# Optimization experiments

Hardware: AMD Instinct MI355X
Metric: run time of the kernel (lower is better)

The kernel has to match this reference:

```python
import jax, jax.numpy as jnp
import numpy as np

DIM = 1024
N_HEADS = 16
HEAD_DIM = DIM // N_HEADS


def setup_inputs() -> dict:
    key = jax.random.key(0)
    ks = jax.random.split(key, 5)
    scale = 1.0 / np.sqrt(DIM)
    x = jax.random.normal(ks[0], (2, 2048, DIM), dtype=jnp.float32)
    W_qkv = jax.random.normal(ks[1], (DIM, 3 * DIM), dtype=jnp.float32) * scale
    b_qkv = jax.random.normal(ks[2], (3 * DIM,), dtype=jnp.float32) * 0.01
    W_proj = jax.random.normal(ks[3], (DIM, DIM), dtype=jnp.float32) * scale
    b_proj = jax.random.normal(ks[4], (DIM,), dtype=jnp.float32) * 0.01
    return {"x": x, "W_qkv": W_qkv, "b_qkv": b_qkv, "W_proj": W_proj, "b_proj": b_proj}


def reference(x, W_qkv, b_qkv, W_proj, b_proj):
    B, T, C = x.shape
    qkv = x @ W_qkv + b_qkv  # [B,T,3C]
    q, k, v = jnp.split(qkv, 3, axis=2)
    # [B,T,C] -> [B,H,T,Dh]
    def heads(y):
        return y.reshape(B, T, N_HEADS, HEAD_DIM).transpose(0, 2, 1, 3)
    q, k, v = heads(q), heads(k), heads(v)
    inv_sqrt_dh = 1.0 / jnp.sqrt(jnp.asarray(HEAD_DIM, dtype=x.dtype))
    attn = jnp.einsum('bhqd,bhkd->bhqk', q, k) * inv_sqrt_dh
    attn = jax.nn.softmax(attn, axis=-1)
    out = jnp.einsum('bhqk,bhkd->bhqd', attn, v)
    out = out.transpose(0, 2, 1, 3).reshape(B, T, C)
    return out @ W_proj + b_proj
```

## Files before the change

kernel.cpp:

```cpp
#include <hip/hip_runtime.h>
#include <hip/hip_bf16.h>
#include <math.h>

using bf16 = __hip_bfloat16;

typedef __bf16 bf16x8 __attribute__((ext_vector_type(8)));
typedef __bf16 bf16x4 __attribute__((ext_vector_type(4)));
typedef float  f32x4  __attribute__((ext_vector_type(4)));
typedef float  f32x16 __attribute__((ext_vector_type(16)));

constexpr int Bb = 2;
constexpr int Ts = 2048;
constexpr int Cc = 1024;
constexpr int Hh = 16;
constexpr int Dh = 64;
constexpr int Mm = Bb * Ts;
constexpr int Nqkv = 3 * Cc;
constexpr int BHTD = Bb * Hh * Ts * Dh;

__device__ __forceinline__
void gll16(const __bf16* g, __bf16* l)
{
    __builtin_amdgcn_global_load_lds(
        (const __attribute__((address_space(1))) unsigned int*)g,
        (__attribute__((address_space(3))) unsigned int*)l,
        16, 0, 0);
}

__global__ __launch_bounds__(256)
void prep_all(const float* __restrict__ x, __bf16* __restrict__ Xb,
              const float* __restrict__ Wq, __bf16* __restrict__ Wqt,
              const float* __restrict__ Wp, __bf16* __restrict__ Wpt)
{
    __shared__ __bf16 tl[64][72];
    const int bid = blockIdx.x;
    const int t = threadIdx.x;

    if (bid < 4096) {
        int i = (bid * 256 + t) * 4;
        float4 v = *(const float4*)(x + i);
        bf16x4 o = { (__bf16)v.x, (__bf16)v.y, (__bf16)v.z, (__bf16)v.w };
        *(bf16x4*)(Xb + i) = o;
        return;
    }
    const float* W; __bf16* Wt; int cols, bx, by;
    if (bid < 4096 + 768) {
        W = Wq; Wt = Wqt; cols = Nqkv;
        bx = (bid - 4096) % 48; by = (bid - 4096) / 48;
    } else {
        W = Wp; Wt = Wpt; cols = Cc;
        bx = (bid - 4864) % 16; by = (bid - 4864) / 16;
    }
    const int c0 = bx * 64;
    const int r0 = by * 64;
    #pragma unroll
    for (int i = 0; i < 4; i++) {
        int e = t + 256 * i;
        int r = e >> 4, c4 = (e & 15) * 4;
        float4 v = *(const float4*)(W + (r0 + r) * cols + c0 + c4);
        bf16x4 o = { (__bf16)v.x, (__bf16)v.y, (__bf16)v.z, (__bf16)v.w };
        *(bf16x4*)&tl[r][c4] = o;
    }
    __syncthreads();
    #pragma unroll
    for (int i = 0; i < 4; i++) {
        int e = t + 256 * i;
        int n = e >> 4, k4 = (e & 15) * 4;
        bf16x4 o = { tl[k4][n], tl[k4 + 1][n], tl[k4 + 2][n], tl[k4 + 3][n] };
        *(bf16x4*)(Wt + (c0 + n) * 1024 + r0 + k4) = o;
    }
}

__device__ __forceinline__
void gemm_core(const __bf16* __restrict__ A, const __bf16* __restrict__ Bt,
               int m0, int n0, int wm, int wn, int quad, int l16, int t,
               f32x4 (&acc)[4][4])
{
    __shared__ __bf16 Al[128][32];
    __shared__ __bf16 Bl[128][32];

    const int wave = t >> 6;
    const int lane = t & 63;
    const int srow = lane >> 2;
    const int scol = (lane & 3) * 8;

    const __bf16* Ag = A  + (size_t)(m0 + wave * 16 + srow) * 1024 + scol;
    const __bf16* Bg = Bt + (size_t)(n0 + wave * 16 + srow) * 1024 + scol;
    __bf16* Al_lo = &Al[wave * 16][0];
    __bf16* Al_hi = &Al[64 + wave * 16][0];
    __bf16* Bl_lo = &Bl[wave * 16][0];
    __bf16* Bl_hi = &Bl[64 + wave * 16][0];

    for (int k0 = 0; k0 < 1024; k0 += 32) {
        gll16(Ag + k0,             Al_lo);
        gll16(Ag + k0 + 64 * 1024, Al_hi);
        gll16(Bg + k0,             Bl_lo);
        gll16(Bg + k0 + 64 * 1024, Bl_hi);
        __syncthreads();
        bf16x8 af[4], bfr[4];
        #pragma unroll
        for (int mt = 0; mt < 4; mt++)
            af[mt] = *(const bf16x8*)&Al[wm * 64 + mt * 16 + l16][quad * 8];
        #pragma unroll
        for (int nt = 0; nt < 4; nt++)
            bfr[nt] = *(const bf16x8*)&Bl[wn * 64 + nt * 16 + l16][quad * 8];
        #pragma unroll
        for (int mt = 0; mt < 4; mt++)
            #pragma unroll
            for (int nt = 0; nt < 4; nt++)
                acc[mt][nt] = __builtin_amdgcn_mfma_f32_16x16x32_bf16(
                    af[mt], bfr[nt], acc[mt][nt], 0, 0, 0);
        __syncthreads();
    }
}

__global__ __launch_bounds__(256)
void qkv_mfma(const __bf16* __restrict__ A, const __bf16* __restrict__ Bt,
              const float* __restrict__ bias, __bf16* __restrict__ qkv)
{
    __shared__ __bf16 ebuf[4][64][72];

    const int t    = threadIdx.x;
    const int wave = t >> 6;
    const int lane = t & 63;
    const int quad = lane >> 4;
    const int l16  = lane & 15;
    const int wm   = wave >> 1, wn = wave & 1;
    const int n0 = blockIdx.x * 128;
    const int m0 = blockIdx.y * 128;

    f32x4 acc[4][4];
    #pragma unroll
    for (int i = 0; i < 4; i++)
        #pragma unroll
        for (int j = 0; j < 4; j++)
            acc[i][j] = f32x4{0.f, 0.f, 0.f, 0.f};

    gemm_core(A, Bt, m0, n0, wm, wn, quad, l16, t, acc);

    const int nw0 = n0 + wn * 64;
    const int which = nw0 >> 10;
    const int h = (nw0 & 1023) >> 6;

    if (which == 2) {
        #pragma unroll
        for (int nt = 0; nt < 4; nt++) {
            int d = nt * 16 + l16;
            float bs = bias[nw0 + nt * 16 + l16];
            #pragma unroll
            for (int mt = 0; mt < 4; mt++) {
                int m = m0 + wm * 64 + mt * 16 + quad * 4;
                int b = m >> 11;
                int tt = m & 2047;
                bf16x4 o = { (__bf16)(acc[mt][nt][0] + bs),
                             (__bf16)(acc[mt][nt][1] + bs),
                             (__bf16)(acc[mt][nt][2] + bs),
                             (__bf16)(acc[mt][nt][3] + bs) };
                *(bf16x4*)&qkv[2 * (size_t)BHTD +
                               (((size_t)(b * 16 + h) * 64 + d) * 2048 + tt)] = o;
            }
        }
    } else {
        #pragma unroll
        for (int nt = 0; nt < 4; nt++) {
            float bs = bias[nw0 + nt * 16 + l16];
            #pragma unroll
            for (int mt = 0; mt < 4; mt++)
                #pragma unroll
                for (int r = 0; r < 4; r++)
                    ebuf[wave][mt * 16 + quad * 4 + r][nt * 16 + l16] =
                        (__bf16)(acc[mt][nt][r] + bs);
        }
        int m = m0 + wm * 64 + lane;
        int b = m >> 11;
        int tt = m & 2047;
        __bf16* dst = &qkv[which * (size_t)BHTD +
                           (((size_t)(b * 16 + h) * 2048 + tt) * 64)];
        #pragma unroll
        for (int c = 0; c < 8; c++)
            *(bf16x8*)(dst + c * 8) = *(const bf16x8*)&ebuf[wave][lane][c * 8];
    }
}

__global__ __launch_bounds__(256)
void proj_mfma(const __bf16* __restrict__ A, const __bf16* __restrict__ Bt,
               const float* __restrict__ bias, float* __restrict__ out)
{
    const int t    = threadIdx.x;
    const int wave = t >> 6;
    const int lane = t & 63;
    const int quad = lane >> 4;
    const int l16  = lane & 15;
    const int wm   = wave >> 1, wn = wave & 1;
    const int n0 = blockIdx.x * 128;
    const int m0 = blockIdx.y * 128;

    f32x4 acc[4][4];
    #pragma unroll
    for (int i = 0; i < 4; i++)
        #pragma unroll
        for (int j = 0; j < 4; j++)
            acc[i][j] = f32x4{0.f, 0.f, 0.f, 0.f};

    gemm_core(A, Bt, m0, n0, wm, wn, quad, l16, t, acc);

    #pragma unroll
    for (int nt = 0; nt < 4; nt++) {
        int n = n0 + wn * 64 + nt * 16 + l16;
        float bs = bias[n];
        #pragma unroll
        for (int mt = 0; mt < 4; mt++) {
            #pragma unroll
            for (int r = 0; r < 4; r++) {
                int m = m0 + wm * 64 + mt * 16 + quad * 4 + r;
                out[m * 1024 + n] = acc[mt][nt][r] + bs;
            }
        }
    }
}

__global__ __launch_bounds__(256, 1)
void attn_mfma(const __bf16* __restrict__ Q, const __bf16* __restrict__ K,
               const __bf16* __restrict__ VT, __bf16* __restrict__ O)
{
    __shared__ __bf16 sK[2][64 * 64];
    __shared__ __bf16 sV[2][64 * 64];

    const int t    = threadIdx.x;
    const int wave = t >> 6;
    const int lane = t & 63;
    const int c    = lane & 31;
    const int hi   = lane >> 5;
    const int hx   = hi * 16;
    const int sw   = (c & 7) << 4;

    const int blk = blockIdx.x;
    const int bh  = blk & 31;
    const int qc  = blk >> 5;
    const int q0  = qc * 256 + wave * 64;

    const __bf16* Qp = Q  + ((size_t)bh * Ts + q0) * Dh;
    const __bf16* Kp = K  + (size_t)bh * Ts * Dh;
    const __bf16* Vp = VT + (size_t)bh * Dh * Ts;

    bf16x8 qf[2][4];
    #pragma unroll
    for (int qs = 0; qs < 2; qs++)
        #pragma unroll
        for (int ds = 0; ds < 4; ds++) {
            bf16x8 v = *(const bf16x8*)(Qp + (qs * 32 + c) * Dh + ds * 16 + hi * 8);
            #pragma unroll
            for (int i = 0; i < 8; i++) v[i] = (__bf16)(0.125f * (float)v[i]);
            qf[qs][ds] = v;
        }

    f32x16 accO[2][2];
    #pragma unroll
    for (int qs = 0; qs < 2; qs++)
        #pragma unroll
        for (int dt = 0; dt < 2; dt++)
            #pragma unroll
            for (int i = 0; i < 16; i++) accO[qs][dt][i] = 0.f;
    float lsum[2] = {0.f, 0.f};

    const int r0 = wave * 8 + (lane >> 3);
    const int s8 = ((lane & 7) ^ (r0 & 7)) * 8;
    const __bf16* kg0 = Kp + r0 * Dh + s8;
    const __bf16* kg1 = Kp + (size_t)(32 + r0) * Dh + s8;
    const __bf16* vg0 = Vp + (size_t)r0 * Ts + s8;
    const __bf16* vg1 = Vp + (size_t)(32 + r0) * Ts + s8;

    gll16(kg0, &sK[0][wave * 512]);
    gll16(kg1, &sK[0][2048 + wave * 512]);
    gll16(vg0, &sV[0][wave * 512]);
    gll16(vg1, &sV[0][2048 + wave * 512]);
    __syncthreads();

    for (int ic = 0; ic < Ts / 64; ic++) {
        const int p = ic & 1;
        if (ic < Ts / 64 - 1) {
            const int pn = p ^ 1;
            gll16(kg0 + (ic + 1) * 4096, &sK[pn][wave * 512]);
            gll16(kg1 + (ic + 1) * 4096, &sK[pn][2048 + wave * 512]);
            gll16(vg0 + (ic + 1) * 64,   &sV[pn][wave * 512]);
            gll16(vg1 + (ic + 1) * 64,   &sV[pn][2048 + wave * 512]);
        }
        const char* kb = (const char*)&sK[p][0];
        const char* vb = (const char*)&sV[p][0];

        bf16x8 kf[2][4];
        #pragma unroll
        for (int kt = 0; kt < 2; kt++) {
            const char* rbase = kb + (kt * 32 + c) * 128;
            #pragma unroll
            for (int ds = 0; ds < 4; ds++)
                kf[kt][ds] = *(const bf16x8*)(rbase + ((ds * 32 + hx) ^ sw));
        }

        f32x16 st[2][2];
        #pragma unroll
        for (int qs = 0; qs < 2; qs++)
            #pragma unroll
            for (int kt = 0; kt < 2; kt++)
                #pragma unroll
                for (int i = 0; i < 16; i++) st[qs][kt][i] = 0.f;
        #pragma unroll
        for (int ds = 0; ds < 4; ds++)
            #pragma unroll
            for (int kt = 0; kt < 2; kt++)
                #pragma unroll
                for (int qs = 0; qs < 2; qs++)
                    st[qs][kt] = __builtin_amdgcn_mfma_f32_32x32x16_bf16(
                        kf[kt][ds], qf[qs][ds], st[qs][kt], 0, 0, 0);

        bf16x8 pa[2][4];
        #pragma unroll
        for (int qs = 0; qs < 2; qs++) {
            unsigned pk[2][8];
            #pragma unroll
            for (int kt = 0; kt < 2; kt++) {
                float sum0 = 0.f, sum1 = 0.f;
                #pragma unroll
                for (int r = 0; r < 16; r++) {
                    float pv = __expf(st[qs][kt][r]);
                    st[qs][kt][r] = pv;
                    if (r & 1) sum1 += pv; else sum0 += pv;
                }
                lsum[qs] += sum0 + sum1;
                #pragma unroll
                for (int r2 = 0; r2 < 8; r2++) {
                    unsigned d;
                    asm("v_cvt_pk_bf16_f32 %0, %1, %2"
                        : "=v"(d)
                        : "v"(st[qs][kt][2 * r2]), "v"(st[qs][kt][2 * r2 + 1]));
                    pk[kt][r2] = d;
                }
            }
            #pragma unroll
            for (int s = 0; s < 4; s++) {
                const int kt = s >> 1, r4 = (s & 1) * 4;
                unsigned x0 = pk[kt][r4 + 0], y0 = pk[kt][r4 + 2];
                unsigned x1 = pk[kt][r4 + 1], y1 = pk[kt][r4 + 3];
                asm("v_permlane32_swap_b32 %0, %1" : "+v"(x0), "+v"(y0));
                asm("v_permlane32_swap_b32 %0, %1" : "+v"(x1), "+v"(y1));
                union { unsigned u[4]; bf16x8 b; } pu;
                pu.u[0] = x0; pu.u[1] = x1; pu.u[2] = y0; pu.u[3] = y1;
                pa[qs][s] = pu.b;
            }
        }

        #pragma unroll
        for (int s = 0; s < 4; s++)
            #pragma unroll
            for (int dt = 0; dt < 2; dt++) {
                bf16x8 vf = *(const bf16x8*)(vb + (dt * 32 + c) * 128 +
                                             ((s * 32 + hx) ^ sw));
                #pragma unroll
                for (int qs = 0; qs < 2; qs++)
                    accO[qs][dt] = __builtin_amdgcn_mfma_f32_32x32x16_bf16(
                        pa[qs][s], vf, accO[qs][dt], 0, 0, 0);
            }
        __syncthreads();
    }

    const int b = bh >> 4, h = bh & 15;
    #pragma unroll
    for (int qs = 0; qs < 2; qs++) {
        float l = lsum[qs] + __shfl_xor(lsum[qs], 32);
        float linv = 1.f / l;
        #pragma unroll
        for (int r = 0; r < 16; r++) {
            const int qrow = (r & 3) + 8 * (r >> 2) + 4 * hi;
            float inv = __shfl(linv, qrow);
            __bf16* Op = O + ((size_t)(b * Ts + q0 + qs * 32 + qrow)) * Cc +
                         h * 64 + c;
            Op[0]  = (__bf16)(accO[qs][0][r] * inv);
            Op[32] = (__bf16)(accO[qs][1][r] * inv);
        }
    }
}

extern "C" void kernel_launch(void* const* d_in, const int* in_sizes, int n_in,
                              void* d_out, int out_size, void* d_ws, size_t ws_size,
                              hipStream_t stream)
{
    (void)in_sizes; (void)n_in; (void)out_size; (void)ws_size;
    const float* x     = (const float*)d_in[0];
    const float* Wqkv  = (const float*)d_in[1];
    const float* bqkv  = (const float*)d_in[2];
    const float* Wproj = (const float*)d_in[3];
    const float* bproj = (const float*)d_in[4];
    float* out = (float*)d_out;

    __bf16* ws   = (__bf16*)d_ws;
    __bf16* Qw   = ws;
    __bf16* XbAO = ws + 3 * (size_t)BHTD;
    __bf16* Wqt  = XbAO + (size_t)Mm * Cc;
    __bf16* Wpt  = Wqt + (size_t)Nqkv * Cc;

    prep_all<<<dim3(5120), 256, 0, stream>>>(x, XbAO, Wqkv, Wqt, Wproj, Wpt);
    qkv_mfma<<<dim3(Nqkv / 128, Mm / 128), 256, 0, stream>>>(XbAO, Wqt, bqkv, Qw);
    attn_mfma<<<dim3(256), 256, 0, stream>>>(
        Qw, Qw + BHTD, Qw + 2 * (size_t)BHTD, XbAO);
    proj_mfma<<<dim3(Cc / 128, Mm / 128), 256, 0, stream>>>(XbAO, Wpt, bproj, out);
}
```

Before: 207.7 us.

## Register-pipeline attention K/V loads from global, shrink proj tile to 64 rows

Attention no longer stages K and V through double-buffered LDS. Each wave now loads K/V fragments straight from global into registers and runs a software-pipelined loop that overlaps the QK, softmax and PV stages across even and odd key blocks. Softmax switches to exp2 with log2e folded into the Q scale, and the per-iteration barriers are removed. The projection GEMM uses 64-row M tiles to double the block count. The trade-off is that each of the four waves now reads K/V from global or L2 on its own instead of sharing one LDS copy, and register pressure rises.

Result: no change. 205.4 us (-1.1%).

```diff
diff --git a/kernel.cpp b/kernel.cpp
--- a/kernel.cpp
+++ b/kernel.cpp
@@ -71,14 +71,16 @@
     }
 }
 
+template<int BM>
 __device__ __forceinline__
 void gemm_core(const __bf16* __restrict__ A, const __bf16* __restrict__ Bt,
                int m0, int n0, int wm, int wn, int quad, int l16, int t,
                f32x4 (&acc)[4][4])
 {
-    __shared__ __bf16 Al[128][32];
+    __shared__ __bf16 Al[BM][32];
     __shared__ __bf16 Bl[128][32];
 
+    constexpr int MT = BM / 32;
     const int wave = t >> 6;
     const int lane = t & 63;
     const int srow = lane >> 2;
@@ -87,25 +89,27 @@
     const __bf16* Ag = A  + (size_t)(m0 + wave * 16 + srow) * 1024 + scol;
     const __bf16* Bg = Bt + (size_t)(n0 + wave * 16 + srow) * 1024 + scol;
     __bf16* Al_lo = &Al[wave * 16][0];
-    __bf16* Al_hi = &Al[64 + wave * 16][0];
     __bf16* Bl_lo = &Bl[wave * 16][0];
     __bf16* Bl_hi = &Bl[64 + wave * 16][0];
 
     for (int k0 = 0; k0 < 1024; k0 += 32) {
-        gll16(Ag + k0,             Al_lo);
-        gll16(Ag + k0 + 64 * 1024, Al_hi);
+        gll16(Ag + k0, Al_lo);
+        if constexpr (BM == 128) {
+            __bf16* Al_hi = &Al[64 + wave * 16][0];
+            gll16(Ag + k0 + 64 * 1024, Al_hi);
+        }
         gll16(Bg + k0,             Bl_lo);
         gll16(Bg + k0 + 64 * 1024, Bl_hi);
         __syncthreads();
-        bf16x8 af[4], bfr[4];
-        #pragma unroll
-        for (int mt = 0; mt < 4; mt++)
-            af[mt] = *(const bf16x8*)&Al[wm * 64 + mt * 16 + l16][quad * 8];
+        bf16x8 af[MT], bfr[4];
+        #pragma unroll
+        for (int mt = 0; mt < MT; mt++)
+            af[mt] = *(const bf16x8*)&Al[wm * (BM / 2) + mt * 16 + l16][quad * 8];
         #pragma unroll
         for (int nt = 0; nt < 4; nt++)
             bfr[nt] = *(const bf16x8*)&Bl[wn * 64 + nt * 16 + l16][quad * 8];
         #pragma unroll
-        for (int mt = 0; mt < 4; mt++)
+        for (int mt = 0; mt < MT; mt++)
             #pragma unroll
             for (int nt = 0; nt < 4; nt++)
                 acc[mt][nt] = __builtin_amdgcn_mfma_f32_16x16x32_bf16(
@@ -136,7 +140,7 @@
         for (int j = 0; j < 4; j++)
             acc[i][j] = f32x4{0.f, 0.f, 0.f, 0.f};
 
-    gemm_core(A, Bt, m0, n0, wm, wn, quad, l16, t, acc);
+    gemm_core<128>(A, Bt, m0, n0, wm, wn, quad, l16, t, acc);
 
     const int nw0 = n0 + wn * 64;
     const int which = nw0 >> 10;
@@ -193,7 +197,7 @@
     const int l16  = lane & 15;
     const int wm   = wave >> 1, wn = wave & 1;
     const int n0 = blockIdx.x * 128;
-    const int m0 = blockIdx.y * 128;
+    const int m0 = blockIdx.y * 64;
 
     f32x4 acc[4][4];
     #pragma unroll
@@ -202,47 +206,129 @@
         for (int j = 0; j < 4; j++)
             acc[i][j] = f32x4{0.f, 0.f, 0.f, 0.f};
 
-    gemm_core(A, Bt, m0, n0, wm, wn, quad, l16, t, acc);
+    gemm_core<64>(A, Bt, m0, n0, wm, wn, quad, l16, t, acc);
 
     #pragma unroll
     for (int nt = 0; nt < 4; nt++) {
         int n = n0 + wn * 64 + nt * 16 + l16;
         float bs = bias[n];
         #pragma unroll
-        for (int mt = 0; mt < 4; mt++) {
+        for (int mt = 0; mt < 2; mt++) {
             #pragma unroll
             for (int r = 0; r < 4; r++) {
-                int m = m0 + wm * 64 + mt * 16 + quad * 4 + r;
+                int m = m0 + wm * 32 + mt * 16 + quad * 4 + r;
                 out[m * 1024 + n] = acc[mt][nt][r] + bs;
             }
         }
     }
+}
+
+__device__ __forceinline__
+void ldk_g(const __bf16* __restrict__ Kb, int j, bf16x8 (&kf)[2][4])
+{
+    #pragma unroll
+    for (int kt = 0; kt < 2; kt++)
+        #pragma unroll
+        for (int ds = 0; ds < 4; ds++)
+            kf[kt][ds] = *(const bf16x8*)(Kb + ((size_t)j * 64 + kt * 32) * 64 + ds * 16);
+}
+
+__device__ __forceinline__
+void ldv_g(const __bf16* __restrict__ Vb, int j, bf16x8 (&vf)[4][2])
+{
+    #pragma unroll
+    for (int s = 0; s < 4; s++)
+        #pragma unroll
+        for (int dt = 0; dt < 2; dt++)
+            vf[s][dt] = *(const bf16x8*)(Vb + (size_t)dt * 32 * Ts + j * 64 + s * 16);
+}
+
+__device__ __forceinline__
+void qk_step(const bf16x8 (&kf)[2][4], const bf16x8 (&qf)[2][4], f32x16 (&st)[2][2])
+{
+    const f32x16 z16 = {0.f, 0.f, 0.f, 0.f, 0.f, 0.f, 0.f, 0.f,
+                        0.f, 0.f, 0.f, 0.f, 0.f, 0.f, 0.f, 0.f};
+    #pragma unroll
+    for (int kt = 0; kt < 2; kt++)
+        #pragma unroll
+        for (int qs = 0; qs < 2; qs++) {
+            f32x16 a;
+            a = __builtin_amdgcn_mfma_f32_32x32x16_bf16(kf[kt][0], qf[qs][0], z16, 0, 0, 0);
+            a = __builtin_amdgcn_mfma_f32_32x32x16_bf16(kf[kt][1], qf[qs][1], a, 0, 0, 0);
+            a = __builtin_amdgcn_mfma_f32_32x32x16_bf16(kf[kt][2], qf[qs][2], a, 0, 0, 0);
+            st[qs][kt] = __builtin_amdgcn_mfma_f32_32x32x16_bf16(kf[kt][3], qf[qs][3], a, 0, 0, 0);
+        }
+}
+
+__device__ __forceinline__
+void sm_step(f32x16 (&st)[2][2], bf16x8 (&pa)[2][4], float (&lsum)[2])
+{
+    #pragma unroll
+    for (int qs = 0; qs < 2; qs++) {
+        #pragma unroll
+        for (int kt = 0; kt < 2; kt++) {
+            float sum0 = 0.f, sum1 = 0.f;
+            #pragma unroll
+            for (int r = 0; r < 16; r++) {
+                float pv = __builtin_amdgcn_exp2f(st[qs][kt][r]);
+                st[qs][kt][r] = pv;
+                if (r & 1) sum1 += pv; else sum0 += pv;
+            }
+            lsum[qs] += sum0 + sum1;
+            #pragma unroll
+            for (int s2 = 0; s2 < 2; s2++) {
+                unsigned pk0, pk1, pk2, pk3;
+                const int r4 = s2 * 8;
+                asm("v_cvt_pk_bf16_f32 %0, %1, %2"
+                    : "=v"(pk0) : "v"(st[qs][kt][r4 + 0]), "v"(st[qs][kt][r4 + 1]));
+                asm("v_cvt_pk_bf16_f32 %0, %1, %2"
+                    : "=v"(pk1) : "v"(st[qs][kt][r4 + 2]), "v"(st[qs][kt][r4 + 3]));
+                asm("v_cvt_pk_bf16_f32 %0, %1, %2"
+                    : "=v"(pk2) : "v"(st[qs][kt][r4 + 4]), "v"(st[qs][kt][r4 + 5]));
+                asm("v_cvt_pk_bf16_f32 %0, %1, %2"
+                    : "=v"(pk3) : "v"(st[qs][kt][r4 + 6]), "v"(st[qs][kt][r4 + 7]));
+                asm("v_permlane32_swap_b32 %0, %1" : "+v"(pk0), "+v"(pk2));
+                asm("v_permlane32_swap_b32 %0, %1" : "+v"(pk1), "+v"(pk3));
+                union { unsigned u[4]; bf16x8 b; } pu;
+                pu.u[0] = pk0; pu.u[1] = pk1; pu.u[2] = pk2; pu.u[3] = pk3;
+                pa[qs][kt * 2 + s2] = pu.b;
+            }
+        }
+    }
+}
+
+__device__ __forceinline__
+void pv_step(const bf16x8 (&pa)[2][4], const bf16x8 (&vf)[4][2], f32x16 (&accO)[2][2])
+{
+    #pragma unroll
+    for (int s = 0; s < 4; s++)
+        #pragma unroll
+        for (int dt = 0; dt < 2; dt++)
+            #pragma unroll
+            for (int qs = 0; qs < 2; qs++)
+                accO[qs][dt] = __builtin_amdgcn_mfma_f32_32x32x16_bf16(
+                    pa[qs][s], vf[s][dt], accO[qs][dt], 0, 0, 0);
 }
 
 __global__ __launch_bounds__(256, 1)
 void attn_mfma(const __bf16* __restrict__ Q, const __bf16* __restrict__ K,
                const __bf16* __restrict__ VT, __bf16* __restrict__ O)
 {
-    __shared__ __bf16 sK[2][64 * 64];
-    __shared__ __bf16 sV[2][64 * 64];
-
     const int t    = threadIdx.x;
     const int wave = t >> 6;
     const int lane = t & 63;
     const int c    = lane & 31;
     const int hi   = lane >> 5;
-    const int hx   = hi * 16;
-    const int sw   = (c & 7) << 4;
 
     const int blk = blockIdx.x;
     const int bh  = blk & 31;
-    const int qc  = blk >> 5;
-    const int q0  = qc * 256 + wave * 64;
+    const int q0  = ((blk >> 5) * 4 + wave) * 64;
 
     const __bf16* Qp = Q  + ((size_t)bh * Ts + q0) * Dh;
-    const __bf16* Kp = K  + (size_t)bh * Ts * Dh;
-    const __bf16* Vp = VT + (size_t)bh * Dh * Ts;
-
+    const __bf16* Kb = K  + (size_t)bh * Ts * Dh + (size_t)c * Dh + hi * 8;
+    const __bf16* Vb = VT + (size_t)bh * Dh * Ts + (size_t)c * Ts + hi * 8;
+
+    const float qscale = 0.125f * 1.44269504088896f;
     bf16x8 qf[2][4];
     #pragma unroll
     for (int qs = 0; qs < 2; qs++)
@@ -250,7 +336,7 @@
         for (int ds = 0; ds < 4; ds++) {
             bf16x8 v = *(const bf16x8*)(Qp + (qs * 32 + c) * Dh + ds * 16 + hi * 8);
             #pragma unroll
-            for (int i = 0; i < 8; i++) v[i] = (__bf16)(0.125f * (float)v[i]);
+            for (int i = 0; i < 8; i++) v[i] = (__bf16)(qscale * (float)v[i]);
             qf[qs][ds] = v;
         }
 
@@ -263,105 +349,34 @@
             for (int i = 0; i < 16; i++) accO[qs][dt][i] = 0.f;
     float lsum[2] = {0.f, 0.f};
 
-    const int r0 = wave * 8 + (lane >> 3);
-    const int s8 = ((lane & 7) ^ (r0 & 7)) * 8;
-    const __bf16* kg0 = Kp + r0 * Dh + s8;
-    const __bf16* kg1 = Kp + (size_t)(32 + r0) * Dh + s8;
-    const __bf16* vg0 = Vp + (size_t)r0 * Ts + s8;
-    const __bf16* vg1 = Vp + (size_t)(32 + r0) * Ts + s8;
-
-    gll16(kg0, &sK[0][wave * 512]);
-    gll16(kg1, &sK[0][2048 + wave * 512]);
-    gll16(vg0, &sV[0][wave * 512]);
-    gll16(vg1, &sV[0][2048 + wave * 512]);
-    __syncthreads();
-
-    for (int ic = 0; ic < Ts / 64; ic++) {
-        const int p = ic & 1;
-        if (ic < Ts / 64 - 1) {
-            const int pn = p ^ 1;
-            gll16(kg0 + (ic + 1) * 4096, &sK[pn][wave * 512]);
-            gll16(kg1 + (ic + 1) * 4096, &sK[pn][2048 + wave * 512]);
-            gll16(vg0 + (ic + 1) * 64,   &sV[pn][wave * 512]);
-            gll16(vg1 + (ic + 1) * 64,   &sV[pn][2048 + wave * 512]);
-        }
-        const char* kb = (const char*)&sK[p][0];
-        const char* vb = (const char*)&sV[p][0];
-
-        bf16x8 kf[2][4];
-        #pragma unroll
-        for (int kt = 0; kt < 2; kt++) {
-            const char* rbase = kb + (kt * 32 + c) * 128;
-            #pragma unroll
-            for (int ds = 0; ds < 4; ds++)
-                kf[kt][ds] = *(const bf16x8*)(rbase + ((ds * 32 + hx) ^ sw));
-        }
-
-        f32x16 st[2][2];
-        #pragma unroll
-        for (int qs = 0; qs < 2; qs++)
-            #pragma unroll
-            for (int kt = 0; kt < 2; kt++)
-                #pragma unroll
-                for (int i = 0; i < 16; i++) st[qs][kt][i] = 0.f;
-        #pragma unroll
-        for (int ds = 0; ds < 4; ds++)
-            #pragma unroll
-            for (int kt = 0; kt < 2; kt++)
-                #pragma unroll
-                for (int qs = 0; qs < 2; qs++)
-                    st[qs][kt] = __builtin_amdgcn_mfma_f32_32x32x16_bf16(
-                        kf[kt][ds], qf[qs][ds], st[qs][kt], 0, 0, 0);
-
-        bf16x8 pa[2][4];
-        #pragma unroll
-        for (int qs = 0; qs < 2; qs++) {
-            unsigned pk[2][8];
-            #pragma unroll
-            for (int kt = 0; kt < 2; kt++) {
-                float sum0 = 0.f, sum1 = 0.f;
-                #pragma unroll
-                for (int r = 0; r < 16; r++) {
-                    float pv = __expf(st[qs][kt][r]);
-                    st[qs][kt][r] = pv;
-                    if (r & 1) sum1 += pv; else sum0 += pv;
-                }
-                lsum[qs] += sum0 + sum1;
-                #pragma unroll
-                for (int r2 = 0; r2 < 8; r2++) {
-                    unsigned d;
-                    asm("v_cvt_pk_bf16_f32 %0, %1, %2"
-                        : "=v"(d)
-                        : "v"(st[qs][kt][2 * r2]), "v"(st[qs][kt][2 * r2 + 1]));
-                    pk[kt][r2] = d;
-                }
-            }
-            #pragma unroll
-            for (int s = 0; s < 4; s++) {
-                const int kt = s >> 1, r4 = (s & 1) * 4;
-                unsigned x0 = pk[kt][r4 + 0], y0 = pk[kt][r4 + 2];
-                unsigned x1 = pk[kt][r4 + 1], y1 = pk[kt][r4 + 3];
-                asm("v_permlane32_swap_b32 %0, %1" : "+v"(x0), "+v"(y0));
-                asm("v_permlane32_swap_b32 %0, %1" : "+v"(x1), "+v"(y1));
-                union { unsigned u[4]; bf16x8 b; } pu;
-                pu.u[0] = x0; pu.u[1] = x1; pu.u[2] = y0; pu.u[3] = y1;
-                pa[qs][s] = pu.b;
-            }
-        }
-
-        #pragma unroll
-        for (int s = 0; s < 4; s++)
-            #pragma unroll
-            for (int dt = 0; dt < 2; dt++) {
-                bf16x8 vf = *(const bf16x8*)(vb + (dt * 32 + c) * 128 +
-                                             ((s * 32 + hx) ^ sw));
-                #pragma unroll
-                for (int qs = 0; qs < 2; qs++)
-                    accO[qs][dt] = __builtin_amdgcn_mfma_f32_32x32x16_bf16(
-                        pa[qs][s], vf, accO[qs][dt], 0, 0, 0);
-            }
-        __syncthreads();
-    }
+    bf16x8 kfE[2][4], kfO[2][4], vfE[4][2], vfO[4][2];
+    f32x16 stE[2][2], stO[2][2];
+    bf16x8 pa[2][4];
+
+    ldk_g(Kb, 0, kfE);
+    qk_step(kfE, qf, stE);
+    ldk_g(Kb, 1, kfO);
+    ldv_g(Vb, 0, vfE);
+
+    for (int i = 0; i < 15; i++) {
+        const int e = 2 * i;
+        ldk_g(Kb, e + 2, kfE);
+        qk_step(kfO, qf, stO);
+        ldv_g(Vb, e + 1, vfO);
+        sm_step(stE, pa, lsum);
+        pv_step(pa, vfE, accO);
+        ldk_g(Kb, e + 3, kfO);
+        qk_step(kfE, qf, stE);
+        ldv_g(Vb, e + 2, vfE);
+        sm_step(stO, pa, lsum);
+        pv_step(pa, vfO, accO);
+    }
+    qk_step(kfO, qf, stO);
+    sm_step(stE, pa, lsum);
+    pv_step(pa, vfE, accO);
+    ldv_g(Vb, 31, vfO);
+    sm_step(stO, pa, lsum);
+    pv_step(pa, vfO, accO);
 
     const int b = bh >> 4, h = bh & 15;
     #pragma unroll
@@ -402,5 +417,5 @@
     qkv_mfma<<<dim3(Nqkv / 128, Mm / 128), 256, 0, stream>>>(XbAO, Wqt, bqkv, Qw);
     attn_mfma<<<dim3(256), 256, 0, stream>>>(
         Qw, Qw + BHTD, Qw + 2 * (size_t)BHTD, XbAO);
-    proj_mfma<<<dim3(Cc / 128, Mm / 128), 256, 0, stream>>>(XbAO, Wpt, bproj, out);
-}
+    proj_mfma<<<dim3(Cc / 128, Mm / 64), 256, 0, stream>>>(XbAO, Wpt, bproj, out);
+}
```
